# Kernel optimization log

Measured on AMD Instinct MI355X. Metric: run time of the kernel, lower is better.

Reference implementation:

```python
import jax, jax.numpy as jnp
import numpy as np

NEG_SLOPE = 0.2  # PyG RGATConv default negative_slope


def _rgat_conv(x, src, dst, edge_type, W, q, k, b, num_nodes):
    # W: [R, in, H] per-relation weight (heads=1 so H = heads*out_channels)
    # Transform every node by every relation once, then gather per edge
    # (same math as PyG's per-edge bmm with index_select'd weights, but
    #  avoids materializing [E, in, H] weights).
    xr = jnp.einsum('ni,rio->rno', x, W)            # [R, N, H]
    qv = jnp.einsum('rno,oh->rnh', xr, q)           # [R, N, heads]
    kv = jnp.einsum('rno,oh->rnh', xr, k)           # [R, N, heads]
    # additive self-attention: alpha_e = leaky_relu(q(out_i) + k(out_j))
    alpha = qv[edge_type, dst] + kv[edge_type, src]  # [E, heads]
    alpha = jnp.where(alpha >= 0, alpha, NEG_SLOPE * alpha)
    # softmax over incoming edges of each destination node (across-relation)
    amax = jax.ops.segment_max(alpha, dst, num_segments=num_nodes)  # [N, heads]
    amax = jnp.where(jnp.isfinite(amax), amax, 0.0)
    ex = jnp.exp(alpha - amax[dst])
    denom = jax.ops.segment_sum(ex, dst, num_segments=num_nodes)
    att = ex / (denom[dst] + 1e-16)                 # [E, heads]
    msg = xr[edge_type, src] * att                  # [E, H] (heads=1 broadcast)
    out = jax.ops.segment_sum(msg, dst, num_segments=num_nodes)    # [N, H]
    return out + b


def setup_inputs() -> dict:
    key = jax.random.key(0)
    ks = jax.random.split(key, 16)
    N, E, R, IN, H = 50000, 800000, 8, 128, 128
    x = jax.random.normal(ks[0], (N, IN), dtype=jnp.float32)
    edge_index = jax.random.randint(ks[1], (2, E), 0, N, dtype=jnp.int32)
    edge_type = jax.random.randint(ks[2], (E,), 0, R, dtype=jnp.int32)
    s_in = 1.0 / np.sqrt(IN)
    s_h = 1.0 / np.sqrt(H)
    w0 = jax.random.normal(ks[3], (R, IN, H), dtype=jnp.float32) * s_in
    q0 = jax.random.normal(ks[4], (H, 1), dtype=jnp.float32) * s_h
    k0 = jax.random.normal(ks[5], (H, 1), dtype=jnp.float32) * s_h
    b0 = jnp.zeros((H,), dtype=jnp.float32)
    w1 = jax.random.normal(ks[6], (R, H, H), dtype=jnp.float32) * s_h
    q1 = jax.random.normal(ks[7], (H, 1), dtype=jnp.float32) * s_h
    k1 = jax.random.normal(ks[8], (H, 1), dtype=jnp.float32) * s_h
    b1 = jnp.zeros((H,), dtype=jnp.float32)
    fc1_w = jax.random.normal(ks[9], (2 * H, H), dtype=jnp.float32) * (1.0 / np.sqrt(2 * H))
    fc1_b = jnp.zeros((H,), dtype=jnp.float32)
    fc2_w = jax.random.normal(ks[10], (H, 1), dtype=jnp.float32) * s_h
    fc2_b = jnp.zeros((1,), dtype=jnp.float32)
    return {"x": x, "edge_index": edge_index, "edge_type": edge_type,
            "w0": w0, "q0": q0, "k0": k0, "b0": b0,
            "w1": w1, "q1": q1, "k1": k1, "b1": b1,
            "fc1_w": fc1_w, "fc1_b": fc1_b, "fc2_w": fc2_w, "fc2_b": fc2_b}


def reference(x, edge_index, edge_type, w0, q0, k0, b0, w1, q1, k1, b1, fc1_w, fc1_b, fc2_w, fc2_b):
    N = x.shape[0]
    src, dst = edge_index[0], edge_index[1]
    h = jax.nn.relu(_rgat_conv(x, src, dst, edge_type, w0, q0, k0, b0, N))
    h = jax.nn.relu(_rgat_conv(h, src, dst, edge_type, w1, q1, k1, b1, N))
    g = jnp.concatenate([h.mean(axis=0), h.max(axis=0)], axis=-1)  # [2H]
    g = jnp.tanh(g)
    g = jax.nn.relu(g @ fc1_w + fc1_b)   # dropout is identity in eval mode
    out = g @ fc2_w + fc2_b              # [1]
    return jax.nn.sigmoid(out)
```

## Files before the change

### kernel.cpp

```cpp
#include <hip/hip_runtime.h>
#include <hip/hip_bf16.h>


typedef __bf16 bf16x8 __attribute__((ext_vector_type(8)));
typedef __bf16 bf16x4 __attribute__((ext_vector_type(4)));
typedef __bf16 bf16x2 __attribute__((ext_vector_type(2)));
typedef float f32x4 __attribute__((ext_vector_type(4)));
typedef float f32x2 __attribute__((ext_vector_type(2)));

#define CBSH 10
#define CSC_CH 4096


__global__ void k_zero(int* __restrict__ p, int n) {
  int i = threadIdx.x;
  if (i < n) p[i] = 0;
}


__global__ __launch_bounds__(256) void k_chist(const int* __restrict__ dst, int* __restrict__ chist, int E) {
  __shared__ int lh[64];
  int t = threadIdx.x;
  if (t < 64) lh[t] = 0;
  __syncthreads();
  for (int e = blockIdx.x * 256 + t; e < E; e += gridDim.x * 256)
    atomicAdd(&lh[dst[e] >> CBSH], 1);
  __syncthreads();
  if (t < 64 && lh[t]) atomicAdd(&chist[t], lh[t]);
}

__global__ __launch_bounds__(256) void k_cscatter(const int* __restrict__ src, const int* __restrict__ dst,
                                                  const int* __restrict__ et, const int* __restrict__ chist,
                                                  int* __restrict__ ccur0, int* __restrict__ tmp, int E) {
  __shared__ int recbuf[CSC_CH];
  __shared__ int lcnt[64], lbase[64], gbase[64], lcur[64], cb[64];
  int t = threadIdx.x;
  int base = blockIdx.x * CSC_CH;
  int cnt = E - base; if (cnt > CSC_CH) cnt = CSC_CH;
  if (t < 64) { lcnt[t] = 0; cb[t] = chist[t]; }
  __syncthreads();
  int myrec[CSC_CH / 256], mycb[CSC_CH / 256];
  int k = 0;
  for (int i = t; i < cnt; i += 256, ++k) {
    int d = dst[base + i];
    int c = d >> CBSH;
    myrec[k] = src[base + i] | (et[base + i] << 17) | ((d & ((1 << CBSH) - 1)) << 20);
    mycb[k] = c;
    atomicAdd(&lcnt[c], 1);
  }
  __syncthreads();
  if (t == 0) {
    int acc = 0, acc2 = 0;
    for (int c = 0; c < 64; ++c) {
      lbase[c] = acc; lcur[c] = acc; acc += lcnt[c];
      int h = cb[c]; cb[c] = acc2; acc2 += h;
    }
  }
  __syncthreads();
  if (t < 64 && lcnt[t] > 0) gbase[t] = cb[t] + atomicAdd(&ccur0[t], lcnt[t]);
  __syncthreads();
  k = 0;
  for (int i = t; i < cnt; i += 256, ++k) {
    int p = atomicAdd(&lcur[mycb[k]], 1);
    recbuf[p] = myrec[k];
  }
  __syncthreads();
  for (int i = t; i < cnt; i += 256) {
    int lo = 0, hi = 63;
    while (lo < hi) { int mid = (lo + hi + 1) >> 1; if (lbase[mid] <= i) lo = mid; else hi = mid - 1; }
    tmp[gbase[lo] + (i - lbase[lo])] = recbuf[i];
  }
}

__global__ __launch_bounds__(1024) void k_fsort(const int* __restrict__ chist, const int* __restrict__ tmp,
                                                int* __restrict__ recs, int* __restrict__ row_ptr,
                                                int N, int E) {
  __shared__ int sd[1024];
  __shared__ int ncur[1024];
  __shared__ int cbs[65];
  int cb = blockIdx.x, t = threadIdx.x;
  int n0 = cb << CBSH;
  if (t < 64) cbs[t] = chist[t];
  __syncthreads();
  if (t == 0) {
    int acc = 0;
    for (int c = 0; c < 64; ++c) { int h = cbs[c]; cbs[c] = acc; acc += h; }
    cbs[64] = acc;
  }
  sd[t] = 0;
  __syncthreads();
  int begin = cbs[cb], endd = cbs[cb + 1];
  for (int i = begin + t; i < endd; i += 1024)
    atomicAdd(&sd[(tmp[i] >> 20) & 1023], 1);
  __syncthreads();
  int myc = sd[t];
  for (int off = 1; off < 1024; off <<= 1) {
    int xv = 0; if (t >= off) xv = sd[t - off];
    __syncthreads();
    sd[t] += xv;
    __syncthreads();
  }
  int ex = sd[t] - myc;
  int node = n0 + t;
  if (node < N) row_ptr[node] = begin + ex;
  if (node == N - 1) row_ptr[N] = E;
  ncur[t] = begin + ex;
  __syncthreads();
  for (int i = begin + t; i < endd; i += 1024) {
    int rc = tmp[i];
    int p = atomicAdd(&ncur[(rc >> 20) & 1023], 1);
    recs[p] = rc & 0xFFFFF;
  }
}


__global__ __launch_bounds__(256) void k_wprep(const float* __restrict__ w0, const float* __restrict__ q0,
                                               const float* __restrict__ k0, const float* __restrict__ w1,
                                               const float* __restrict__ q1, const float* __restrict__ k1,
                                               __bf16* __restrict__ wqkb, __bf16* __restrict__ WT) {
  int layer, bx = blockIdx.x;
  if (bx >= 384) { layer = 1; bx -= 384; } else layer = 0;
  const float* W = layer ? w1 : w0;
  const float* q = layer ? q1 : q0;
  const float* k = layer ? k1 : k0;
  __bf16* wq = wqkb + layer * 2048;
  __bf16* WTl = WT + (size_t)layer * 131072;
  if (bx < 256) {
    int g = bx * 4 + (threadIdx.x >> 6);
    int lane = threadIdx.x & 63;
    const float2* wrow = (const float2*)(W + (size_t)g * 128);
    float2 wv = wrow[lane];
    float2 qv2 = ((const float2*)q)[lane];
    float2 kv2 = ((const float2*)k)[lane];
    float aq = wv.x * qv2.x + wv.y * qv2.y;
    float ak = wv.x * kv2.x + wv.y * kv2.y;
    #pragma unroll
    for (int off = 32; off; off >>= 1) {
      aq += __shfl_xor(aq, off, 64);
      ak += __shfl_xor(ak, off, 64);
    }
    if (lane == 0) { wq[g] = (__bf16)aq; wq[1024 + g] = (__bf16)ak; }
  } else {
    __shared__ float t[32][33];
    int bb = bx - 256;
    int r = bb >> 4;
    int rem = bb & 15;
    int kk0 = (rem & 3) * 32, h0 = (rem >> 2) * 32;
    int tx = threadIdx.x & 31;
    int ty = threadIdx.x >> 5;
    #pragma unroll
    for (int i = 0; i < 4; ++i) {
      int kk = ty + i * 8;
      t[kk][tx] = W[((size_t)r * 128 + kk0 + kk) * 128 + h0 + tx];
    }
    __syncthreads();
    #pragma unroll
    for (int i = 0; i < 4; ++i) {
      int hh = ty + i * 8;
      WTl[(size_t)(h0 + hh) * 1024 + r * 128 + kk0 + tx] = (__bf16)t[tx][hh];
    }
  }
}


#define ASTR 136

template <int L0>
__global__ __launch_bounds__(256) void k_gemmY(const void* __restrict__ xin,
                                               const __bf16* __restrict__ WT2,
                                               const __bf16* __restrict__ wqkb,
                                               unsigned char* __restrict__ Y, float* __restrict__ qkv, int M) {
  __shared__ __bf16 As[128 * ASTR];
  __shared__ __bf16 Bs[128 * ASTR];
  int bm = blockIdx.x * 128;
  int tid = threadIdx.x;
  int w = tid >> 6, l = tid & 63;
  int srow = tid >> 1;
  int cb8 = (tid & 1) * 8;
  bool valid = (bm + srow) < M;

  if (L0) {
    const float* gA = (const float*)xin + (size_t)(bm + srow) * 128 + cb8 * 8;
    #pragma unroll
    for (int i = 0; i < 8; ++i) {
      float4 f0 = make_float4(0.f, 0.f, 0.f, 0.f), f1 = f0;
      if (valid) { f0 = *(const float4*)(gA + i * 8); f1 = *(const float4*)(gA + i * 8 + 4); }
      bf16x8 v;
      v[0] = (__bf16)f0.x; v[1] = (__bf16)f0.y; v[2] = (__bf16)f0.z; v[3] = (__bf16)f0.w;
      v[4] = (__bf16)f1.x; v[5] = (__bf16)f1.y; v[6] = (__bf16)f1.z; v[7] = (__bf16)f1.w;
      *(bf16x8*)&As[srow * ASTR + (cb8 + i) * 8] = v;
    }
  } else {
    const bf16x8* gA = (const bf16x8*)((const __bf16*)xin + (size_t)(bm + srow) * 128);
    #pragma unroll
    for (int i = 0; i < 8; ++i) {
      bf16x8 v = valid ? gA[cb8 + i] : (bf16x8)(__bf16)0.0f;
      *(bf16x8*)&As[srow * ASTR + (cb8 + i) * 8] = v;
    }
  }
  {
    int qr = tid >> 4, qc = tid & 15;
    *(bf16x8*)&Bs[qr * ASTR + qc * 8] = *(const bf16x8*)(wqkb + (size_t)qr * 128 + qc * 8);
  }
  __syncthreads();

  {
    f32x4 qacc[2];
    qacc[0] = (f32x4)0.f; qacc[1] = (f32x4)0.f;
    #pragma unroll
    for (int ks = 0; ks < 4; ++ks) {
      bf16x8 bq = *(const bf16x8*)&Bs[(l & 15) * ASTR + ks * 32 + (l >> 4) * 8];
      #pragma unroll
      for (int m2 = 0; m2 < 2; ++m2) {
        bf16x8 af = *(const bf16x8*)&As[(w * 32 + m2 * 16 + (l & 15)) * ASTR + ks * 32 + (l >> 4) * 8];
        qacc[m2] = __builtin_amdgcn_mfma_f32_16x16x32_bf16(af, bq, qacc[m2], 0, 0, 0);
      }
    }
    #pragma unroll
    for (int m2 = 0; m2 < 2; ++m2)
      #pragma unroll
      for (int j = 0; j < 4; ++j) {
        int row = w * 32 + m2 * 16 + (l >> 4) * 4 + j;
        if (bm + row < M) qkv[(size_t)(bm + row) * 16 + (l & 15)] = qacc[m2][j];
      }
  }

  for (int r = 0; r < 8; ++r) {
    __syncthreads();
    {
      const bf16x8* gB = (const bf16x8*)(WT2 + (size_t)srow * 1024 + r * 128);
      #pragma unroll
      for (int i = 0; i < 8; ++i)
        *(bf16x8*)&Bs[srow * ASTR + (cb8 + i) * 8] = gB[cb8 + i];
    }
    __syncthreads();

    f32x4 acc[2][8];
    #pragma unroll
    for (int m2 = 0; m2 < 2; ++m2)
      #pragma unroll
      for (int n2 = 0; n2 < 8; ++n2) acc[m2][n2] = (f32x4)0.f;

    #pragma unroll
    for (int ks = 0; ks < 4; ++ks) {
      bf16x8 af[2], bfv[8];
      #pragma unroll
      for (int m2 = 0; m2 < 2; ++m2)
        af[m2] = *(const bf16x8*)&As[(w * 32 + m2 * 16 + (l & 15)) * ASTR + ks * 32 + (l >> 4) * 8];
      #pragma unroll
      for (int n2 = 0; n2 < 8; ++n2)
        bfv[n2] = *(const bf16x8*)&Bs[(n2 * 16 + (l & 15)) * ASTR + ks * 32 + (l >> 4) * 8];
      #pragma unroll
      for (int m2 = 0; m2 < 2; ++m2)
        #pragma unroll
        for (int n2 = 0; n2 < 8; ++n2)
          acc[m2][n2] = __builtin_amdgcn_mfma_f32_16x16x32_bf16(af[m2], bfv[n2], acc[m2][n2], 0, 0, 0);
    }

    unsigned char* Yr = Y + ((size_t)r * M + bm) * 128;
    #pragma unroll
    for (int m2 = 0; m2 < 2; ++m2)
      #pragma unroll
      for (int j = 0; j < 4; ++j) {
        int row = w * 32 + m2 * 16 + (l >> 4) * 4 + j;
        if (bm + row < M) {
          int pk0 = __builtin_amdgcn_cvt_pk_fp8_f32(acc[m2][0][j], acc[m2][1][j], 0, false);
          pk0 = __builtin_amdgcn_cvt_pk_fp8_f32(acc[m2][2][j], acc[m2][3][j], pk0, true);
          int pk1 = __builtin_amdgcn_cvt_pk_fp8_f32(acc[m2][4][j], acc[m2][5][j], 0, false);
          pk1 = __builtin_amdgcn_cvt_pk_fp8_f32(acc[m2][6][j], acc[m2][7][j], pk1, true);
          *(int2*)(Yr + (size_t)row * 128 + (l & 15) * 8) = make_int2(pk0, pk1);
        }
      }
  }
}


__global__ __launch_bounds__(256) void k_aggY(const int* __restrict__ row_ptr, const int* __restrict__ recs,
                                              const float* __restrict__ qkv, const unsigned char* __restrict__ Y,
                                              const float* __restrict__ bias, __bf16* __restrict__ hout,
                                              int N) {
  int wv = threadIdx.x >> 6;
  int lane = threadIdx.x & 63;
  int n = blockIdx.x * 4 + wv;
  if (n >= N) return;
  int start = row_ptr[n], end = row_ptr[n + 1];
  const float* qvn = qkv + (size_t)n * 16;
  float denom = 0.f, m_run = -1e30f;
  int sub = lane & 15;
  int grp = lane >> 4;
  float acc[8];
  #pragma unroll
  for (int j = 0; j < 8; ++j) acc[j] = 0.f;

  for (int c0 = start; c0 < end; c0 += 64) {
    int cend = (end < c0 + 64) ? end : (c0 + 64);
    int cnt = cend - c0;
    int p = c0 + lane;
    float a = -1e30f; int rec = 0;
    if (p < cend) {
      rec = recs[p];
      int s = rec & 0x1FFFF, r = (rec >> 17) & 7;
      float t = qvn[r] + qkv[(size_t)s * 16 + 8 + r];
      a = (t >= 0.f) ? t : 0.2f * t;
    }
    float cm = a;
    #pragma unroll
    for (int off = 32; off; off >>= 1) cm = fmaxf(cm, __shfl_xor(cm, off, 64));
    if (cm > m_run) {
      if (m_run > -1e29f) {
        float scale = __expf(m_run - cm);
        denom *= scale;
        #pragma unroll
        for (int j = 0; j < 8; ++j) acc[j] *= scale;
      }
      m_run = cm;
    }
    float wgt = (p < cend) ? __expf(a - m_run) : 0.f;
    float ws = wgt;
    #pragma unroll
    for (int off = 32; off; off >>= 1) ws += __shfl_xor(ws, off, 64);
    denom += ws;
    int wbits = __float_as_int(wgt);

    int nbatch = (cnt + 3) >> 2;
    #pragma unroll 2
    for (int b = 0; b < nbatch; ++b) {
      int idx = grp * 4 + b * 16;
      int rg = __builtin_amdgcn_ds_bpermute(idx, rec);
      int wg = __builtin_amdgcn_ds_bpermute(idx, wbits);
      float fw = __int_as_float(wg);
      int s_ = rg & 0x1FFFF;
      int r_ = (rg >> 17) & 7;
      int2 xv = *(const int2*)(Y + (((size_t)r_ * N + s_) << 7) + sub * 8);
      f32x2 f01 = __builtin_amdgcn_cvt_pk_f32_fp8(xv.x, false);
      f32x2 f23 = __builtin_amdgcn_cvt_pk_f32_fp8(xv.x, true);
      f32x2 f45 = __builtin_amdgcn_cvt_pk_f32_fp8(xv.y, false);
      f32x2 f67 = __builtin_amdgcn_cvt_pk_f32_fp8(xv.y, true);
      acc[0] += fw * f01[0]; acc[1] += fw * f01[1];
      acc[2] += fw * f23[0]; acc[3] += fw * f23[1];
      acc[4] += fw * f45[0]; acc[5] += fw * f45[1];
      acc[6] += fw * f67[0]; acc[7] += fw * f67[1];
    }
  }

  #pragma unroll
  for (int j = 0; j < 8; ++j) {
    acc[j] += __shfl_xor(acc[j], 16, 64);
    acc[j] += __shfl_xor(acc[j], 32, 64);
  }
  float inv = 1.f / (denom + 1e-16f);
  if (grp == 0) {
    #pragma unroll
    for (int j = 0; j < 8; ++j) {
      float v = fmaxf(acc[j] * inv + bias[j * 16 + sub], 0.f);
      hout[(size_t)n * 128 + j * 16 + sub] = (__bf16)v;
    }
  }
}


__global__ __launch_bounds__(256) void k_pool(const __bf16* __restrict__ h, float* __restrict__ gsum,
                                              float* __restrict__ gmax, int N) {
  int c2 = threadIdx.x & 63;
  int grp = threadIdx.x >> 6;
  float s0 = 0.f, s1 = 0.f, m0 = 0.f, m1 = 0.f;
  for (int n = blockIdx.x * 4 + grp; n < N; n += gridDim.x * 4) {
    bf16x2 v = ((const bf16x2*)(h + (size_t)n * 128))[c2];
    float v0 = (float)v.x, v1 = (float)v.y;
    s0 += v0; s1 += v1;
    m0 = fmaxf(m0, v0); m1 = fmaxf(m1, v1);
  }
  __shared__ float ss0[256], ss1[256], sm0[256], sm1[256];
  ss0[threadIdx.x] = s0; ss1[threadIdx.x] = s1;
  sm0[threadIdx.x] = m0; sm1[threadIdx.x] = m1;
  __syncthreads();
  if (grp == 0) {
    #pragma unroll
    for (int g = 1; g < 4; ++g) {
      s0 += ss0[g * 64 + c2]; s1 += ss1[g * 64 + c2];
      m0 = fmaxf(m0, sm0[g * 64 + c2]); m1 = fmaxf(m1, sm1[g * 64 + c2]);
    }
    atomicAdd(&gsum[2 * c2 + 0], s0);
    atomicAdd(&gsum[2 * c2 + 1], s1);
    atomicMax((int*)gmax + 2 * c2 + 0, __float_as_int(m0));
    atomicMax((int*)gmax + 2 * c2 + 1, __float_as_int(m1));
  }
}

__global__ void k_head(const float* __restrict__ gsum, const float* __restrict__ gmax,
                       const float* __restrict__ fc1w, const float* __restrict__ fc1b,
                       const float* __restrict__ fc2w, const float* __restrict__ fc2b,
                       float* __restrict__ out, int N) {
  __shared__ float g[256];
  __shared__ float red[128];
  int t = threadIdx.x;
  if (t < 128) g[t] = tanhf(gsum[t] / (float)N);
  else g[t] = tanhf(gmax[t - 128]);
  __syncthreads();
  float r1 = 0.f;
  if (t < 128) {
    float a = fc1b[t];
    for (int i = 0; i < 256; i++) a += g[i] * fc1w[i * 128 + t];
    r1 = a > 0.f ? a : 0.f;
    red[t] = r1 * fc2w[t];
  }
  __syncthreads();
  for (int s = 64; s > 0; s >>= 1) {
    if (t < s) red[t] += red[t + s];
    __syncthreads();
  }
  if (t == 0) {
    float o = red[0] + fc2b[0];
    out[0] = 1.f / (1.f + __expf(-o));
  }
}


extern "C" void kernel_launch(void* const* d_in, const int* in_sizes, int n_in,
                              void* d_out, int out_size, void* d_ws, size_t ws_size,
                              hipStream_t stream) {
  const float* x    = (const float*)d_in[0];
  const int*   ei   = (const int*)d_in[1];
  const int*   ety  = (const int*)d_in[2];
  const float* w0   = (const float*)d_in[3];
  const float* q0   = (const float*)d_in[4];
  const float* k0   = (const float*)d_in[5];
  const float* b0   = (const float*)d_in[6];
  const float* w1   = (const float*)d_in[7];
  const float* q1   = (const float*)d_in[8];
  const float* k1   = (const float*)d_in[9];
  const float* b1   = (const float*)d_in[10];
  const float* fc1w = (const float*)d_in[11];
  const float* fc1b = (const float*)d_in[12];
  const float* fc2w = (const float*)d_in[13];
  const float* fc2b = (const float*)d_in[14];
  int N = in_sizes[0] / 128;
  int E = in_sizes[2];
  const int* src = ei;
  const int* dst = ei + E;

  char* base = (char*)d_ws;
  size_t off = 0;
  auto alloc = [&](size_t bytes) -> void* {
    off = (off + 255) & ~(size_t)255;
    void* p = base + off;
    off += bytes;
    return p;
  };
  int ncb = (N + (1 << CBSH) - 1) >> CBSH;

  int*    row_ptr = (int*)alloc((size_t)(N + 1) * 4);
  int*    ctrl    = (int*)alloc(384 * 4);
  int*    chist   = ctrl;
  int*    ccur0   = ctrl + 64;
  float*  gpool   = (float*)(ctrl + 128);
  float*  gsum    = gpool;
  float*  gmax    = gpool + 128;
  int*    tmp     = (int*)alloc((size_t)E * 4);
  int*    recs    = (int*)alloc((size_t)E * 4);
  float*  qkv     = (float*)alloc((size_t)N * 16 * 4);
  __bf16* wqkb    = (__bf16*)alloc(2 * 2048 * 2);
  __bf16* h1b     = (__bf16*)alloc((size_t)N * 128 * 2);
  __bf16* h2b     = (__bf16*)alloc((size_t)N * 128 * 2);
  __bf16* WT2     = (__bf16*)alloc((size_t)2 * 131072 * 2);
  unsigned char* Y = (unsigned char*)alloc((size_t)8 * N * 128);

  k_zero<<<1, 384, 0, stream>>>(ctrl, 384);
  k_chist<<<256, 256, 0, stream>>>(dst, chist, E);
  k_cscatter<<<(E + CSC_CH - 1) / CSC_CH, 256, 0, stream>>>(src, dst, ety, chist, ccur0, tmp, E);
  k_fsort<<<ncb, 1024, 0, stream>>>(chist, tmp, recs, row_ptr, N, E);

  k_wprep<<<768, 256, 0, stream>>>(w0, q0, k0, w1, q1, k1, wqkb, WT2);

  for (int layer = 0; layer < 2; ++layer) {
    const float* bb   = layer ? b1 : b0;
    __bf16*      hout = layer ? h2b : h1b;
    if (layer == 0)
      k_gemmY<1><<<(N + 127) / 128, 256, 0, stream>>>((const void*)x, WT2, wqkb, Y, qkv, N);
    else
      k_gemmY<0><<<(N + 127) / 128, 256, 0, stream>>>((const void*)h1b, WT2 + 131072, wqkb + 2048, Y, qkv, N);
    k_aggY<<<(N + 3) / 4, 256, 0, stream>>>(row_ptr, recs, qkv, Y, bb, hout, N);
  }

  k_pool<<<256, 256, 0, stream>>>(h2b, gsum, gmax, N);
  k_head<<<1, 256, 0, stream>>>(gsum, gmax, fc1w, fc1b, fc2w, fc2b, (float*)d_out, N);
}
```

Baseline: 223.1 us.

## Load GEMM B operands directly from global and keep A fragments in registers

The shared-memory staging buffer for the weight tiles is removed. Each wave now reads its B fragments straight from global memory (through the caches) for every relation, and its A fragments are loaded from LDS once into registers and reused across all 8 relations. This drops the two block barriers per relation and halves LDS use, which may raise occupancy. In exchange each wave issues redundant global loads of the weight tile, and the register-held A fragments add register pressure.

```diff
diff --git a/kernel.cpp b/kernel.cpp
--- a/kernel.cpp
+++ b/kernel.cpp
@@ -171,7 +171,6 @@
                                                const __bf16* __restrict__ wqkb,
                                                unsigned char* __restrict__ Y, float* __restrict__ qkv, int M) {
   __shared__ __bf16 As[128 * ASTR];
-  __shared__ __bf16 Bs[128 * ASTR];
   int bm = blockIdx.x * 128;
   int tid = threadIdx.x;
   int w = tid >> 6, l = tid & 63;
@@ -198,23 +197,24 @@
       *(bf16x8*)&As[srow * ASTR + (cb8 + i) * 8] = v;
     }
   }
-  {
-    int qr = tid >> 4, qc = tid & 15;
-    *(bf16x8*)&Bs[qr * ASTR + qc * 8] = *(const bf16x8*)(wqkb + (size_t)qr * 128 + qc * 8);
-  }
-  __syncthreads();
+  __syncthreads();
+
+  bf16x8 afr[2][4];
+  #pragma unroll
+  for (int m2 = 0; m2 < 2; ++m2)
+    #pragma unroll
+    for (int ks = 0; ks < 4; ++ks)
+      afr[m2][ks] = *(const bf16x8*)&As[(w * 32 + m2 * 16 + (l & 15)) * ASTR + ks * 32 + (l >> 4) * 8];
 
   {
     f32x4 qacc[2];
     qacc[0] = (f32x4)0.f; qacc[1] = (f32x4)0.f;
     #pragma unroll
     for (int ks = 0; ks < 4; ++ks) {
-      bf16x8 bq = *(const bf16x8*)&Bs[(l & 15) * ASTR + ks * 32 + (l >> 4) * 8];
+      bf16x8 bq = *(const bf16x8*)(wqkb + (size_t)(l & 15) * 128 + ks * 32 + (l >> 4) * 8);
       #pragma unroll
-      for (int m2 = 0; m2 < 2; ++m2) {
-        bf16x8 af = *(const bf16x8*)&As[(w * 32 + m2 * 16 + (l & 15)) * ASTR + ks * 32 + (l >> 4) * 8];
-        qacc[m2] = __builtin_amdgcn_mfma_f32_16x16x32_bf16(af, bq, qacc[m2], 0, 0, 0);
-      }
+      for (int m2 = 0; m2 < 2; ++m2)
+        qacc[m2] = __builtin_amdgcn_mfma_f32_16x16x32_bf16(afr[m2][ks], bq, qacc[m2], 0, 0, 0);
     }
     #pragma unroll
     for (int m2 = 0; m2 < 2; ++m2)
@@ -226,15 +226,6 @@
   }
 
   for (int r = 0; r < 8; ++r) {
-    __syncthreads();
-    {
-      const bf16x8* gB = (const bf16x8*)(WT2 + (size_t)srow * 1024 + r * 128);
-      #pragma unroll
-      for (int i = 0; i < 8; ++i)
-        *(bf16x8*)&Bs[srow * ASTR + (cb8 + i) * 8] = gB[cb8 + i];
-    }
-    __syncthreads();
-
     f32x4 acc[2][8];
     #pragma unroll
     for (int m2 = 0; m2 < 2; ++m2)
@@ -243,18 +234,13 @@
 
     #pragma unroll
     for (int ks = 0; ks < 4; ++ks) {
-      bf16x8 af[2], bfv[8];
       #pragma unroll
-      for (int m2 = 0; m2 < 2; ++m2)
-        af[m2] = *(const bf16x8*)&As[(w * 32 + m2 * 16 + (l & 15)) * ASTR + ks * 32 + (l >> 4) * 8];
-      #pragma unroll
-      for (int n2 = 0; n2 < 8; ++n2)
-        bfv[n2] = *(const bf16x8*)&Bs[(n2 * 16 + (l & 15)) * ASTR + ks * 32 + (l >> 4) * 8];
-      #pragma unroll
-      for (int m2 = 0; m2 < 2; ++m2)
+      for (int n2 = 0; n2 < 8; ++n2) {
+        bf16x8 bv = *(const bf16x8*)(WT2 + (size_t)(n2 * 16 + (l & 15)) * 1024 + r * 128 + ks * 32 + (l >> 4) * 8);
         #pragma unroll
-        for (int n2 = 0; n2 < 8; ++n2)
-          acc[m2][n2] = __builtin_amdgcn_mfma_f32_16x16x32_bf16(af[m2], bfv[n2], acc[m2][n2], 0, 0, 0);
+        for (int m2 = 0; m2 < 2; ++m2)
+          acc[m2][n2] = __builtin_amdgcn_mfma_f32_16x16x32_bf16(afr[m2][ks], bv, acc[m2][n2], 0, 0, 0);
+      }
     }
 
     unsigned char* Yr = Y + ((size_t)r * M + bm) * 128;
```

After: 296.1 us. +32.8%, slower.
